# Optimization experiments

Hardware: AMD Instinct MI355X
Metric: run time of the kernel (lower is better)

Reference implementation:

```python
import jax, jax.numpy as jnp
import numpy as np

E = 200_000       # num edges
A = 1_000_000     # num angle triplets
H = 128           # hidden_dim
BD = 8            # bilinear_dim
NR = 6            # num_radial_basis
NS = 7            # num_spherical_basis
MIN = 128         # message_in_dim
N_BEFORE = 1
N_AFTER = 2


def setup_inputs() -> dict:
    key = jax.random.key(0)
    ks = jax.random.split(key, 24)
    s = 0.05
    inp = {
        "distance_representation": jax.random.normal(ks[0], (E, NR), jnp.float32),
        "angle_representation": jax.random.normal(ks[1], (A, NS, NR), jnp.float32),
        "message": jax.random.normal(ks[2], (E, MIN), jnp.float32),
        "angle_index": jax.random.randint(ks[3], (2, A), 0, E),
        # parameters (stored as [in, out]; torch Linear applies x @ W.T)
        "W_dist": jax.random.normal(ks[4], (NR, H), jnp.float32) * s,
        "W_angle": jax.random.normal(ks[5], (NS * NR, BD), jnp.float32) * s,
        "W_src": jax.random.normal(ks[6], (MIN, H), jnp.float32) * s,
        "b_src": jnp.zeros((H,), jnp.float32),
        "W_tgt": jax.random.normal(ks[7], (MIN, H), jnp.float32) * s,
        "b_tgt": jnp.zeros((H,), jnp.float32),
        "W_bil": jax.random.normal(ks[8], (H, BD, H), jnp.float32) * (2.0 / H),
        "res_before_W": jax.random.normal(ks[9], (N_BEFORE, 2, H, H), jnp.float32) * s,
        "res_before_b": jnp.zeros((N_BEFORE, 2, H), jnp.float32),
        "W_skip": jax.random.normal(ks[10], (H, MIN), jnp.float32) * s,
        "b_skip": jnp.zeros((MIN,), jnp.float32),
        "res_after_W": jax.random.normal(ks[11], (N_AFTER, 2, MIN, MIN), jnp.float32) * s,
        "res_after_b": jnp.zeros((N_AFTER, 2, MIN), jnp.float32),
    }
    return inp


def _residual(x, Ws, bs, act):
    # x + act(L2(act(L1(x))))
    h = act(x @ Ws[0] + bs[0])
    h = act(h @ Ws[1] + bs[1])
    return x + h


def reference(distance_representation, angle_representation, message, angle_index,
              W_dist, W_angle, W_src, b_src, W_tgt, b_tgt, W_bil,
              res_before_W, res_before_b, W_skip, b_skip,
              res_after_W, res_after_b):
    act = jax.nn.silu
    num_edges = message.shape[0]
    num_angles = angle_index.shape[-1]

    d = distance_representation @ W_dist                       # [E, H]
    a = angle_representation.reshape(num_angles, -1) @ W_angle  # [A, BD]

    src_e, tgt_e = angle_index[0], angle_index[1]
    sm = message[src_e] @ W_src + b_src                        # [A, H] gather + linear
    sm = sm * d[tgt_e]                                         # [A, H]
    sm = jnp.einsum('ab,ah,ibh->ai', a, sm, W_bil)             # [A, H] bilinear

    agg = jax.ops.segment_sum(sm, tgt_e, num_segments=num_edges)  # [E, H] scatter-add

    x0 = message
    x = agg + (message @ W_tgt + b_tgt)
    for i in range(res_before_W.shape[0]):
        x = _residual(x, res_before_W[i], res_before_b[i], act)
    x = act(x @ W_skip + b_skip) + x0
    for i in range(res_after_W.shape[0]):
        x = _residual(x, res_after_W[i], res_after_b[i], act)
    return x
```

## Files before the change

### kernel.cpp

```cpp
#include <hip/hip_runtime.h>
#include <hip/hip_fp16.h>
#include <stdint.h>

#define E_N 200000
#define A_N 1000000

typedef short s16x8 __attribute__((ext_vector_type(8)));
typedef short s16x4 __attribute__((ext_vector_type(4)));
typedef float f32x4 __attribute__((ext_vector_type(4)));
typedef uint32_t u32x4 __attribute__((ext_vector_type(4)));
typedef uint32_t u32x2 __attribute__((ext_vector_type(2)));
typedef _Float16 f16x8 __attribute__((ext_vector_type(8)));

__device__ __forceinline__ ushort f2bf(float f) {
  uint32_t x = __float_as_uint(f);
  uint32_t r = x + 0x7FFFu + ((x >> 16) & 1u);
  return (ushort)(r >> 16);
}

__device__ __forceinline__ ushort f2h(float f) {
  return __half_as_ushort(__float2half(f));
}

__device__ __forceinline__ uint32_t cvtpk(float lo, float hi) {
  uint32_t r;
  asm("v_cvt_pk_bf16_f32 %0, %1, %2" : "=v"(r) : "v"(lo), "v"(hi));
  return r;
}

__device__ __forceinline__ uint32_t pkmul(uint32_t a, uint32_t b) {
  uint32_t r;
  asm("v_pk_mul_f16 %0, %1, %2" : "=v"(r) : "v"(a), "v"(b));
  return r;
}

__device__ __forceinline__ float silu_f(float v) {
  return v * (1.0f / (1.0f + __expf(-v)));
}

__device__ __forceinline__ int swz(int row, int h) {
  return row * 128 + (h ^ ((row & 7) << 3));
}

__device__ __forceinline__ int sws(int r, int c) {
  return r * 64 + ((c & 63) ^ ((r & 7) << 3));
}

__device__ __forceinline__ void exchCtoB(ushort* scw, int r15, int hi,
                                         const f32x4* xv, s16x8* st) {
  u32x2 pk[8];
#pragma unroll
  for (int nt = 0; nt < 8; nt++) {
    pk[nt][0] = cvtpk(xv[nt][0], xv[nt][1]);
    pk[nt][1] = cvtpk(xv[nt][2], xv[nt][3]);
  }
#pragma unroll
  for (int nt = 0; nt < 4; nt++)
    *(u32x2*)&scw[sws(r15, nt * 16 + hi * 4)] = pk[nt];
#pragma unroll
  for (int k = 0; k < 2; k++)
    st[k] = *(const s16x8*)&scw[sws(r15, k * 32 + hi * 8)];
#pragma unroll
  for (int nt = 4; nt < 8; nt++)
    *(u32x2*)&scw[sws(r15, nt * 16 + hi * 4)] = pk[nt];
#pragma unroll
  for (int k = 2; k < 4; k++)
    st[k] = *(const s16x8*)&scw[sws(r15, k * 32 + hi * 8)];
}

__device__ __forceinline__ void exchBtoC(ushort* scw, int r15, int hi,
                                         const s16x8* stv, u32x2* mc) {
#pragma unroll
  for (int k = 0; k < 2; k++)
    *(s16x8*)&scw[sws(r15, k * 32 + hi * 8)] = stv[k];
#pragma unroll
  for (int nt = 0; nt < 4; nt++)
    mc[nt] = *(const u32x2*)&scw[sws(r15, nt * 16 + hi * 4)];
#pragma unroll
  for (int k = 2; k < 4; k++)
    *(s16x8*)&scw[sws(r15, k * 32 + hi * 8)] = stv[k];
#pragma unroll
  for (int nt = 4; nt < 8; nt++)
    mc[nt] = *(const u32x2*)&scw[sws(r15, nt * 16 + hi * 4)];
}

__global__ __launch_bounds__(256) void k_prep(
    const float* __restrict__ Wbil, const float* __restrict__ Wsrc,
    const float* __restrict__ Wtgt, const float* __restrict__ WresB,
    const float* __restrict__ Wskip, const float* __restrict__ WresA,
    const float* __restrict__ bsrc, const float* __restrict__ btgt,
    const float* __restrict__ bresB, const float* __restrict__ bskip,
    const float* __restrict__ bresA,
    ushort* __restrict__ wg_bil, ushort* __restrict__ wg_lin,
    float* __restrict__ bias_tab) {
  int tid = blockIdx.x * 256 + threadIdx.x;
  if (tid < 8 * 16384) {
    int b = tid >> 14, r = tid & 16383;
    int i = r >> 7, h = r & 127;
    wg_bil[b * 16384 + swz(i, h)] = f2h(Wbil[(i * 8 + b) * 128 + h]);
    return;
  }
  tid -= 8 * 16384;
  if (tid < 9 * 16384) {
    int s = tid >> 14, r = tid & 16383;
    int c = r >> 7, h = r & 127;
    const float* src;
    switch (s) {
      case 0: src = Wsrc; break;
      case 1: src = Wtgt; break;
      case 2: src = WresB; break;
      case 3: src = WresB + 16384; break;
      case 4: src = Wskip; break;
      case 5: src = WresA; break;
      case 6: src = WresA + 16384; break;
      case 7: src = WresA + 32768; break;
      default: src = WresA + 49152; break;
    }
    wg_lin[s * 16384 + swz(c, h)] = f2bf(src[h * 128 + c]);
    return;
  }
  tid -= 9 * 16384;
  if (tid < 9 * 128) {
    int s = tid >> 7, c = tid & 127;
    const float* src;
    switch (s) {
      case 0: src = bsrc; break;
      case 1: src = btgt; break;
      case 2: src = bresB; break;
      case 3: src = bresB + 128; break;
      case 4: src = bskip; break;
      case 5: src = bresA; break;
      case 6: src = bresA + 128; break;
      case 7: src = bresA + 256; break;
      default: src = bresA + 384; break;
    }
    bias_tab[s * 128 + c] = src[c];
  }
}

__global__ __launch_bounds__(256) void k_hist(const int* __restrict__ aidx,
                                              int* __restrict__ cnt) {
  int i = blockIdx.x * 256 + threadIdx.x;
  if (i < A_N) atomicAdd(&cnt[aidx[A_N + i]], 1);
}

__global__ __launch_bounds__(256) void k_scan1(const int* __restrict__ cnt,
                                               int* __restrict__ excl,
                                               int* __restrict__ bsum) {
  __shared__ int s[256];
  int t = threadIdx.x;
  int base = blockIdx.x * 1024 + t * 4;
  int v[4];
#pragma unroll
  for (int j = 0; j < 4; j++) v[j] = (base + j < E_N) ? cnt[base + j] : 0;
  int sum = v[0] + v[1] + v[2] + v[3];
  s[t] = sum;
  __syncthreads();
#pragma unroll
  for (int d = 1; d < 256; d <<= 1) {
    int x = (t >= d) ? s[t - d] : 0;
    __syncthreads();
    s[t] += x;
    __syncthreads();
  }
  int run = s[t] - sum;
#pragma unroll
  for (int j = 0; j < 4; j++) {
    if (base + j < E_N) excl[base + j] = run;
    run += v[j];
  }
  if (t == 255) bsum[blockIdx.x] = s[255];
}

__global__ __launch_bounds__(256) void k_scan2(int* __restrict__ bsum, int nb) {
  __shared__ int s[256];
  int t = threadIdx.x;
  int orig = (t < nb) ? bsum[t] : 0;
  s[t] = orig;
  __syncthreads();
#pragma unroll
  for (int d = 1; d < 256; d <<= 1) {
    int x = (t >= d) ? s[t - d] : 0;
    __syncthreads();
    s[t] += x;
    __syncthreads();
  }
  if (t < nb) bsum[t] = s[t] - orig;
}

__global__ __launch_bounds__(256) void k_scan3(const int* __restrict__ excl,
                                               const int* __restrict__ bsum,
                                               int* __restrict__ cursor) {
  int t = threadIdx.x;
  int base = blockIdx.x * 1024 + t * 4;
  int add = bsum[blockIdx.x];
#pragma unroll
  for (int j = 0; j < 4; j++)
    if (base + j < E_N) cursor[base + j] = excl[base + j] + add;
}

__global__ __launch_bounds__(256) void k_scatter(const int* __restrict__ aidx,
                                                 int* __restrict__ cursor,
                                                 int* __restrict__ perm,
                                                 int* __restrict__ ste) {
  int i = blockIdx.x * 256 + threadIdx.x;
  if (i < A_N) {
    int te = aidx[A_N + i];
    int pos = atomicAdd(&cursor[te], 1);
    perm[pos] = i;
    ste[pos] = te;
  }
}

__global__ __launch_bounds__(256) void k_angle(const float* __restrict__ ang,
                                               const float* __restrict__ Wang,
                                               float* __restrict__ a_ws) {
  __shared__ float rows[128 * 42];
  __shared__ float wbuf[42 * 8];
  int t = threadIdx.x;
  int tile0 = blockIdx.x * 128;
  int nrows = A_N - tile0; if (nrows > 128) nrows = 128;
  if (nrows == 128) {
    const f32x4* src = (const f32x4*)(ang + (size_t)tile0 * 42);
    f32x4* dst = (f32x4*)rows;
    for (int k = t; k < 1344; k += 256) dst[k] = src[k];
  } else {
    int cnt = nrows * 42;
    for (int k = t; k < cnt; k += 256) rows[k] = ang[(size_t)tile0 * 42 + k];
  }
  for (int k = t; k < 336; k += 256) wbuf[k] = Wang[k];
  __syncthreads();
  int row = t >> 1, half = t & 1;
  if (row < nrows) {
    float a0 = 0.f, a1 = 0.f, a2 = 0.f, a3 = 0.f;
    const float* rp = &rows[row * 42];
    const float* wp = &wbuf[half * 4];
#pragma unroll
    for (int k = 0; k < 42; k++) {
      float v = rp[k];
      a0 += v * wp[k * 8 + 0]; a1 += v * wp[k * 8 + 1];
      a2 += v * wp[k * 8 + 2]; a3 += v * wp[k * 8 + 3];
    }
    f32x4 o; o.x = a0; o.y = a1; o.z = a2; o.w = a3;
    *(f32x4*)&a_ws[(tile0 + row) * 8 + half * 4] = o;
  }
}

__global__ __launch_bounds__(256) void k_dist(const float* __restrict__ dist,
                                              const float* __restrict__ Wd,
                                              ushort* __restrict__ dtab) {
  __shared__ float w[6 * 128];
  int t = threadIdx.x;
  for (int k = t; k < 768; k += 256) w[k] = Wd[k];
  __syncthreads();
  int gid = blockIdx.x * 256 + t;
  int e = gid >> 2, q = gid & 3;
  if (e >= E_N) return;
  float dv[6];
#pragma unroll
  for (int r = 0; r < 6; r++) dv[r] = dist[e * 6 + r];
#pragma unroll
  for (int j = 0; j < 32; j += 4) {
    int c = q * 32 + j;
    s16x4 o;
#pragma unroll
    for (int jj = 0; jj < 4; jj++) {
      float s = 0.f;
#pragma unroll
      for (int r = 0; r < 6; r++) s += dv[r] * w[r * 128 + c + jj];
      o[jj] = (short)f2h(s);
    }
    *(s16x4*)&dtab[e * 128 + c] = o;
  }
}

__global__ __launch_bounds__(512) void k_srcm(const float* __restrict__ msg,
                                              const ushort* __restrict__ wg_lin,
                                              const float* __restrict__ bias_tab,
                                              ushort* __restrict__ srcm) {
  __shared__ ushort xb[128 * 128];
  __shared__ ushort wb[16384];
  __shared__ float bias[128];
  int t = threadIdx.x;
  int tile0 = blockIdx.x * 128;
  const f32x4 Z4 = {0.f, 0.f, 0.f, 0.f};
  for (int off = t * 8; off < 16384; off += 4096)
    *(s16x8*)&wb[off] = *(const s16x8*)&wg_lin[off];
  if (t < 128) bias[t] = bias_tab[t];
  {
    int row = t >> 2, l = t & 3;
    int grow = tile0 + row;
#pragma unroll
    for (int j = 0; j < 8; j++) {
      int h = l * 32 + j * 4;
      s16x4 o; o[0] = 0; o[1] = 0; o[2] = 0; o[3] = 0;
      if (grow < E_N) {
        f32x4 v = *(const f32x4*)&msg[(size_t)grow * 128 + h];
        o[0] = (short)f2bf(v.x); o[1] = (short)f2bf(v.y);
        o[2] = (short)f2bf(v.z); o[3] = (short)f2bf(v.w);
      }
      *(s16x4*)&xb[swz(row, h)] = o;
    }
  }
  __syncthreads();
  int w = t >> 6, lane = t & 63;
  int rbase = w * 16;
  int arow = rbase + (lane & 15);
  int k0 = (lane >> 4) * 8;
  int r0 = (lane >> 4) * 4;
  f32x4 acc[8];
#pragma unroll
  for (int k = 0; k < 4; k++) {
    s16x8 af = *(const s16x8*)&xb[swz(arow, k * 32 + k0)];
#pragma unroll
    for (int nt = 0; nt < 8; nt++) {
      s16x8 bf = *(const s16x8*)&wb[swz(nt * 16 + (lane & 15), k * 32 + k0)];
      acc[nt] = __builtin_amdgcn_mfma_f32_16x16x32_bf16(af, bf, k == 0 ? Z4 : acc[nt], 0, 0, 0);
    }
  }
#pragma unroll
  for (int nt = 0; nt < 8; nt++) {
    int col = nt * 16 + (lane & 15);
    float bv = bias[col];
#pragma unroll
    for (int r = 0; r < 4; r++) {
      int grow = tile0 + rbase + r0 + r;
      if (grow < E_N) srcm[(size_t)grow * 128 + col] = f2h(acc[nt][r] + bv);
    }
  }
}

__global__ __launch_bounds__(256, 3) void k_bil(const int* __restrict__ aidx,
                                                const ushort* __restrict__ srcm,
                                                const ushort* __restrict__ dtab,
                                                const float* __restrict__ a_ws,
                                                const ushort* __restrict__ wg_bil,
                                                const int* __restrict__ perm,
                                                const int* __restrict__ ste,
                                                float* __restrict__ agg) {
  __shared__ ushort wb[16384];
  int t = threadIdx.x;
  int lane = t & 63, w = t >> 6;
  int bid = blockIdx.x;
  int xcd = bid & 7, jj0 = bid >> 3;
  int swb = (xcd < 5 ? xcd * 977 : 5 * 977 + (xcd - 5) * 976) + jj0;
  int tile0 = swb * 128;
  int mb = w * 32;
  int r15 = lane & 15, hi = lane >> 4;
  int k0 = hi * 8;
  int r0 = hi * 4;
  const f32x4 Z4 = {0.f, 0.f, 0.f, 0.f};

  {
    const ushort* gs = wg_bil + w * 4096 + lane * 8;
    ushort* ls = &wb[w * 4096];
#pragma unroll
    for (int i = 0; i < 8; i++)
      __builtin_amdgcn_global_load_lds(
          (const __attribute__((address_space(1))) void*)(gs + i * 512),
          (__attribute__((address_space(3))) void*)(ls + i * 512), 16, 0, 0);
  }

  u32x4 smv[2][4];
  uint32_t avd[2][8];
  int teo[2][4];
#pragma unroll
  for (int mt = 0; mt < 2; mt++) {
    int grow = tile0 + mb + mt * 16 + r15;
    int ok = (grow < A_N);
    int ga = ok ? perm[grow] : 0;
    int se = ok ? aidx[ga] : 0;
    int te = ok ? ste[grow] : 0;
    if (ok) {
      f32x4 a0 = *(const f32x4*)&a_ws[(size_t)ga * 8];
      f32x4 a1 = *(const f32x4*)&a_ws[(size_t)ga * 8 + 4];
#pragma unroll
      for (int j = 0; j < 4; j++) {
        uint32_t h0 = f2h(a0[j]), h1 = f2h(a1[j]);
        avd[mt][j] = (h0 << 16) | h0;
        avd[mt][4 + j] = (h1 << 16) | h1;
      }
    } else {
#pragma unroll
      for (int j = 0; j < 8; j++) avd[mt][j] = 0u;
    }
#pragma unroll
    for (int k = 0; k < 4; k++) {
      u32x4 sv = *(const u32x4*)&srcm[(size_t)se * 128 + k * 32 + k0];
      u32x4 dv = *(const u32x4*)&dtab[(size_t)te * 128 + k * 32 + k0];
#pragma unroll
      for (int j = 0; j < 4; j++) smv[mt][k][j] = pkmul(sv[j], dv[j]);
    }
#pragma unroll
    for (int r = 0; r < 4; r++) {
      int orow = tile0 + mb + mt * 16 + r0 + r;
      teo[mt][r] = (orow < A_N) ? ste[orow] : 0;
    }
  }

  f32x4 OUT[2][8];
#pragma unroll
  for (int mt = 0; mt < 2; mt++)
#pragma unroll
    for (int nt = 0; nt < 8; nt++) OUT[mt][nt] = Z4;

  __syncthreads();

#pragma unroll
  for (int b = 0; b < 8; b++) {
    uint32_t a0b = avd[0][b], a1b = avd[1][b];
    __builtin_amdgcn_s_setprio(1);
#pragma unroll
    for (int k = 0; k < 4; k++) {
      u32x4 p0, p1;
#pragma unroll
      for (int j = 0; j < 4; j++) {
        p0[j] = pkmul(smv[0][k][j], a0b);
        p1[j] = pkmul(smv[1][k][j], a1b);
      }
      f16x8 af0 = __builtin_bit_cast(f16x8, p0);
      f16x8 af1 = __builtin_bit_cast(f16x8, p1);
#pragma unroll
      for (int nt = 0; nt < 8; nt++) {
        f16x8 bf = *(const f16x8*)&wb[swz(nt * 16 + r15, k * 32 + k0)];
        OUT[0][nt] = __builtin_amdgcn_mfma_f32_16x16x32_f16(af0, bf, OUT[0][nt], 0, 0, 0);
        OUT[1][nt] = __builtin_amdgcn_mfma_f32_16x16x32_f16(af1, bf, OUT[1][nt], 0, 0, 0);
      }
    }
    __builtin_amdgcn_s_setprio(0);
    if (b < 7) {
      __syncthreads();
      const ushort* gs = wg_bil + (b + 1) * 16384 + w * 4096 + lane * 8;
      ushort* ls = &wb[w * 4096];
#pragma unroll
      for (int i = 0; i < 8; i++)
        __builtin_amdgcn_global_load_lds(
            (const __attribute__((address_space(1))) void*)(gs + i * 512),
            (__attribute__((address_space(3))) void*)(ls + i * 512), 16, 0, 0);
      __syncthreads();
    }
  }

#pragma unroll
  for (int mt = 0; mt < 2; mt++) {
    float acc[8];
    int cte = teo[mt][0];
#pragma unroll
    for (int nt = 0; nt < 8; nt++) acc[nt] = OUT[mt][nt][0];
#pragma unroll
    for (int r = 1; r < 4; r++) {
      int nte = teo[mt][r];
      if (nte == cte) {
#pragma unroll
        for (int nt = 0; nt < 8; nt++) acc[nt] += OUT[mt][nt][r];
      } else {
        float* base = &agg[(size_t)cte * 128];
#pragma unroll
        for (int nt = 0; nt < 8; nt++)
          unsafeAtomicAdd(base + nt * 16 + r15, acc[nt]);
        cte = nte;
#pragma unroll
        for (int nt = 0; nt < 8; nt++) acc[nt] = OUT[mt][nt][r];
      }
    }
    float* base = &agg[(size_t)cte * 128];
#pragma unroll
    for (int nt = 0; nt < 8; nt++)
      unsafeAtomicAdd(base + nt * 16 + r15, acc[nt]);
  }
}

__global__ __launch_bounds__(512) void k_postA(const float* __restrict__ msg,
                                               const float* __restrict__ agg,
                                               const ushort* __restrict__ wg_lin,
                                               const float* __restrict__ bias_tab,
                                               ushort* __restrict__ xmid) {
  __shared__ ushort wb[4][16384];
  __shared__ ushort sc[8][1024];
  __shared__ float bias[4][128];
  int t = threadIdx.x;
  int lane = t & 63, w = t >> 6;
  int r15 = lane & 15, hi = lane >> 4;
  ushort* scw = &sc[w][0];
  const f32x4 Z4 = {0.f, 0.f, 0.f, 0.f};

#pragma unroll
  for (int s = 0; s < 4; s++) {
    const ushort* gs = wg_lin + (s + 1) * 16384 + t * 8;
    ushort* ls = &wb[s][t * 8];
#pragma unroll
    for (int i = 0; i < 4; i++)
      __builtin_amdgcn_global_load_lds(
          (const __attribute__((address_space(1))) void*)(gs + i * 4096),
          (__attribute__((address_space(3))) void*)(ls + i * 4096), 16, 0, 0);
  }
  if (t < 128) {
#pragma unroll
    for (int s = 0; s < 4; s++) bias[s][t] = bias_tab[(s + 1) * 128 + t];
  }
  __syncthreads();

#pragma unroll 1
  for (int tb = blockIdx.x; tb < 1563; tb += 256) {
    int r = tb * 128 + w * 16 + r15;
    bool ok = r < E_N;
    size_t gb = (size_t)r * 128;

    s16x8 st[4], mg[4];
#pragma unroll
    for (int k = 0; k < 4; k++) {
      f32x4 v0 = Z4, v1 = Z4;
      if (ok) {
        v0 = *(const f32x4*)&msg[gb + k * 32 + hi * 8];
        v1 = *(const f32x4*)&msg[gb + k * 32 + hi * 8 + 4];
      }
      u32x4 p;
      p[0] = cvtpk(v0.x, v0.y); p[1] = cvtpk(v0.z, v0.w);
      p[2] = cvtpk(v1.x, v1.y); p[3] = cvtpk(v1.z, v1.w);
      st[k] = __builtin_bit_cast(s16x8, p);
      mg[k] = st[k];
    }
    f32x4 ag[8];
#pragma unroll
    for (int nt = 0; nt < 8; nt++)
      ag[nt] = ok ? *(const f32x4*)&agg[gb + nt * 16 + hi * 4] : Z4;

    f32x4 xr[8], xv[8], C[8];

#pragma unroll
    for (int k = 0; k < 4; k++)
#pragma unroll
      for (int nt = 0; nt < 8; nt++) {
        s16x8 af = *(const s16x8*)&wb[0][swz(nt * 16 + r15, k * 32 + hi * 8)];
        C[nt] = __builtin_amdgcn_mfma_f32_16x16x32_bf16(af, st[k], k == 0 ? ag[nt] : C[nt], 0, 0, 0);
      }
#pragma unroll
    for (int nt = 0; nt < 8; nt++) {
      f32x4 bv = *(const f32x4*)&bias[0][nt * 16 + hi * 4];
#pragma unroll
      for (int q = 0; q < 4; q++) xv[nt][q] = C[nt][q] + bv[q];
      xr[nt] = xv[nt];
    }
    exchCtoB(scw, r15, hi, xv, st);

#pragma unroll
    for (int k = 0; k < 4; k++)
#pragma unroll
      for (int nt = 0; nt < 8; nt++) {
        s16x8 af = *(const s16x8*)&wb[1][swz(nt * 16 + r15, k * 32 + hi * 8)];
        C[nt] = __builtin_amdgcn_mfma_f32_16x16x32_bf16(af, st[k], k == 0 ? Z4 : C[nt], 0, 0, 0);
      }
#pragma unroll
    for (int nt = 0; nt < 8; nt++) {
      f32x4 bv = *(const f32x4*)&bias[1][nt * 16 + hi * 4];
#pragma unroll
      for (int q = 0; q < 4; q++) xv[nt][q] = silu_f(C[nt][q] + bv[q]);
    }
    exchCtoB(scw, r15, hi, xv, st);

#pragma unroll
    for (int k = 0; k < 4; k++)
#pragma unroll
      for (int nt = 0; nt < 8; nt++) {
        s16x8 af = *(const s16x8*)&wb[2][swz(nt * 16 + r15, k * 32 + hi * 8)];
        C[nt] = __builtin_amdgcn_mfma_f32_16x16x32_bf16(af, st[k], k == 0 ? Z4 : C[nt], 0, 0, 0);
      }
#pragma unroll
    for (int nt = 0; nt < 8; nt++) {
      f32x4 bv = *(const f32x4*)&bias[2][nt * 16 + hi * 4];
#pragma unroll
      for (int q = 0; q < 4; q++) xv[nt][q] = xr[nt][q] + silu_f(C[nt][q] + bv[q]);
    }
    exchCtoB(scw, r15, hi, xv, st);

#pragma unroll
    for (int k = 0; k < 4; k++)
#pragma unroll
      for (int nt = 0; nt < 8; nt++) {
        s16x8 af = *(const s16x8*)&wb[3][swz(nt * 16 + r15, k * 32 + hi * 8)];
        C[nt] = __builtin_amdgcn_mfma_f32_16x16x32_bf16(af, st[k], k == 0 ? Z4 : C[nt], 0, 0, 0);
      }
    u32x2 mc[8];
    exchBtoC(scw, r15, hi, mg, mc);
#pragma unroll
    for (int nt = 0; nt < 8; nt++) {
      f32x4 bv = *(const f32x4*)&bias[3][nt * 16 + hi * 4];
      f32x4 m0;
      m0[0] = __uint_as_float(mc[nt][0] << 16);
      m0[1] = __uint_as_float(mc[nt][0] & 0xffff0000u);
      m0[2] = __uint_as_float(mc[nt][1] << 16);
      m0[3] = __uint_as_float(mc[nt][1] & 0xffff0000u);
      u32x2 pk;
      float o0 = silu_f(C[nt][0] + bv[0]) + m0[0];
      float o1 = silu_f(C[nt][1] + bv[1]) + m0[1];
      float o2 = silu_f(C[nt][2] + bv[2]) + m0[2];
      float o3 = silu_f(C[nt][3] + bv[3]) + m0[3];
      pk[0] = cvtpk(o0, o1);
      pk[1] = cvtpk(o2, o3);
      if (ok) *(u32x2*)&xmid[gb + nt * 16 + hi * 4] = pk;
    }
  }
}

__global__ __launch_bounds__(512) void k_postB(const ushort* __restrict__ xmid,
                                               const ushort* __restrict__ wg_lin,
                                               const float* __restrict__ bias_tab,
                                               float* __restrict__ xout) {
  __shared__ ushort wb[4][16384];
  __shared__ ushort sc[8][1024];
  __shared__ float bias[4][128];
  int t = threadIdx.x;
  int lane = t & 63, w = t >> 6;
  int r15 = lane & 15, hi = lane >> 4;
  ushort* scw = &sc[w][0];
  const f32x4 Z4 = {0.f, 0.f, 0.f, 0.f};

#pragma unroll
  for (int s = 0; s < 4; s++) {
    const ushort* gs = wg_lin + (s + 5) * 16384 + t * 8;
    ushort* ls = &wb[s][t * 8];
#pragma unroll
    for (int i = 0; i < 4; i++)
      __builtin_amdgcn_global_load_lds(
          (const __attribute__((address_space(1))) void*)(gs + i * 4096),
          (__attribute__((address_space(3))) void*)(ls + i * 4096), 16, 0, 0);
  }
  if (t < 128) {
#pragma unroll
    for (int s = 0; s < 4; s++) bias[s][t] = bias_tab[(s + 5) * 128 + t];
  }
  __syncthreads();

#pragma unroll 1
  for (int tb = blockIdx.x; tb < 1563; tb += 256) {
    int r = tb * 128 + w * 16 + r15;
    bool ok = r < E_N;
    size_t gb = (size_t)r * 128;

    s16x8 st[4];
#pragma unroll
    for (int k = 0; k < 4; k++) {
      s16x8 z; u32x4 zz; zz[0] = 0; zz[1] = 0; zz[2] = 0; zz[3] = 0;
      z = __builtin_bit_cast(s16x8, zz);
      st[k] = ok ? *(const s16x8*)&xmid[gb + k * 32 + hi * 8] : z;
    }
    u32x2 mc[8];
    exchBtoC(scw, r15, hi, st, mc);
    f32x4 xr[8], xv[8], C[8];
#pragma unroll
    for (int nt = 0; nt < 8; nt++) {
      xr[nt][0] = __uint_as_float(mc[nt][0] << 16);
      xr[nt][1] = __uint_as_float(mc[nt][0] & 0xffff0000u);
      xr[nt][2] = __uint_as_float(mc[nt][1] << 16);
      xr[nt][3] = __uint_as_float(mc[nt][1] & 0xffff0000u);
    }

#pragma unroll
    for (int k = 0; k < 4; k++)
#pragma unroll
      for (int nt = 0; nt < 8; nt++) {
        s16x8 af = *(const s16x8*)&wb[0][swz(nt * 16 + r15, k * 32 + hi * 8)];
        C[nt] = __builtin_amdgcn_mfma_f32_16x16x32_bf16(af, st[k], k == 0 ? Z4 : C[nt], 0, 0, 0);
      }
#pragma unroll
    for (int nt = 0; nt < 8; nt++) {
      f32x4 bv = *(const f32x4*)&bias[0][nt * 16 + hi * 4];
#pragma unroll
      for (int q = 0; q < 4; q++) xv[nt][q] = silu_f(C[nt][q] + bv[q]);
    }
    exchCtoB(scw, r15, hi, xv, st);

#pragma unroll
    for (int k = 0; k < 4; k++)
#pragma unroll
      for (int nt = 0; nt < 8; nt++) {
        s16x8 af = *(const s16x8*)&wb[1][swz(nt * 16 + r15, k * 32 + hi * 8)];
        C[nt] = __builtin_amdgcn_mfma_f32_16x16x32_bf16(af, st[k], k == 0 ? Z4 : C[nt], 0, 0, 0);
      }
#pragma unroll
    for (int nt = 0; nt < 8; nt++) {
      f32x4 bv = *(const f32x4*)&bias[1][nt * 16 + hi * 4];
#pragma unroll
      for (int q = 0; q < 4; q++) xv[nt][q] = xr[nt][q] + silu_f(C[nt][q] + bv[q]);
      xr[nt] = xv[nt];
    }
    exchCtoB(scw, r15, hi, xv, st);

#pragma unroll
    for (int k = 0; k < 4; k++)
#pragma unroll
      for (int nt = 0; nt < 8; nt++) {
        s16x8 af = *(const s16x8*)&wb[2][swz(nt * 16 + r15, k * 32 + hi * 8)];
        C[nt] = __builtin_amdgcn_mfma_f32_16x16x32_bf16(af, st[k], k == 0 ? Z4 : C[nt], 0, 0, 0);
      }
#pragma unroll
    for (int nt = 0; nt < 8; nt++) {
      f32x4 bv = *(const f32x4*)&bias[2][nt * 16 + hi * 4];
#pragma unroll
      for (int q = 0; q < 4; q++) xv[nt][q] = silu_f(C[nt][q] + bv[q]);
    }
    exchCtoB(scw, r15, hi, xv, st);

#pragma unroll
    for (int k = 0; k < 4; k++)
#pragma unroll
      for (int nt = 0; nt < 8; nt++) {
        s16x8 af = *(const s16x8*)&wb[3][swz(nt * 16 + r15, k * 32 + hi * 8)];
        C[nt] = __builtin_amdgcn_mfma_f32_16x16x32_bf16(af, st[k], k == 0 ? Z4 : C[nt], 0, 0, 0);
      }
#pragma unroll
    for (int nt = 0; nt < 8; nt++) {
      f32x4 bv = *(const f32x4*)&bias[3][nt * 16 + hi * 4];
      f32x4 o;
#pragma unroll
      for (int q = 0; q < 4; q++) o[q] = xr[nt][q] + silu_f(C[nt][q] + bv[q]);
      if (ok) *(f32x4*)&xout[gb + nt * 16 + hi * 4] = o;
    }
  }
}

extern "C" void kernel_launch(void* const* d_in, const int* in_sizes, int n_in,
                              void* d_out, int out_size, void* d_ws, size_t ws_size,
                              hipStream_t stream) {
  const float* dist  = (const float*)d_in[0];
  const float* ang   = (const float*)d_in[1];
  const float* msg   = (const float*)d_in[2];
  const int*   aidx  = (const int*)d_in[3];
  const float* Wd    = (const float*)d_in[4];
  const float* Wang  = (const float*)d_in[5];
  const float* Wsrc  = (const float*)d_in[6];
  const float* bsrc  = (const float*)d_in[7];
  const float* Wtgt  = (const float*)d_in[8];
  const float* btgt  = (const float*)d_in[9];
  const float* Wbil  = (const float*)d_in[10];
  const float* WresB = (const float*)d_in[11];
  const float* bresB = (const float*)d_in[12];
  const float* Wskip = (const float*)d_in[13];
  const float* bskip = (const float*)d_in[14];
  const float* WresA = (const float*)d_in[15];
  const float* bresA = (const float*)d_in[16];

  char* ws = (char*)d_ws;
  ushort* srcm_f16 = (ushort*)(ws + 0);
  ushort* dtab_f16 = (ushort*)(ws + 51200000LL);
  float*  a_ws     = (float*)(ws + 102400000LL);
  ushort* wg_bil   = (ushort*)(ws + 134400000LL);
  ushort* wg_lin   = (ushort*)(ws + 134662144LL);
  float*  bias_tab = (float*)(ws + 134957056LL);
  int*    cnt      = (int*)(ws + 134961664LL);
  int*    cursor   = (int*)(ws + 135761664LL);
  int*    excl     = (int*)(ws + 136561664LL);
  int*    bsum     = (int*)(ws + 137361664LL);
  int*    perm     = (int*)(ws + 137362688LL);
  int*    ste      = (int*)(ws + 141362688LL);
  ushort* xmid     = (ushort*)(ws + 145362688LL);
  float*  agg      = (float*)d_out;

  (void)in_sizes; (void)n_in; (void)out_size; (void)ws_size;

  const int NSCAN = (E_N + 1023) / 1024;

  hipMemsetAsync(d_out, 0, (size_t)E_N * 128 * 4, stream);
  hipMemsetAsync(cnt, 0, (size_t)E_N * 4, stream);
  k_prep<<<1093, 256, 0, stream>>>(Wbil, Wsrc, Wtgt, WresB, Wskip, WresA,
                                   bsrc, btgt, bresB, bskip, bresA,
                                   wg_bil, wg_lin, bias_tab);
  k_hist<<<3907, 256, 0, stream>>>(aidx, cnt);
  k_scan1<<<NSCAN, 256, 0, stream>>>(cnt, excl, bsum);
  k_scan2<<<1, 256, 0, stream>>>(bsum, NSCAN);
  k_scan3<<<NSCAN, 256, 0, stream>>>(excl, bsum, cursor);
  k_scatter<<<3907, 256, 0, stream>>>(aidx, cursor, perm, ste);
  k_angle<<<7813, 256, 0, stream>>>(ang, Wang, a_ws);
  k_dist<<<3125, 256, 0, stream>>>(dist, Wd, dtab_f16);
  k_srcm<<<1563, 512, 0, stream>>>(msg, wg_lin, bias_tab, srcm_f16);
  k_bil<<<7813, 256, 0, stream>>>(aidx, srcm_f16, dtab_f16, a_ws, wg_bil,
                                  perm, ste, agg);
  k_postA<<<256, 512, 0, stream>>>(msg, agg, wg_lin, bias_tab, xmid);
  k_postB<<<256, 512, 0, stream>>>(xmid, wg_lin, bias_tab, (float*)d_out);
}
```

Baseline: 795.2 us.

## Pre-sort angle coefficients and source indices into tgt-sorted order before bilinear

The scatter kernel now also writes the source edge index in sorted order. A new k_asort kernel gathers the angle projection through perm and stores it pre-converted to packed fp16 in sorted order. k_bil then reads sse and a_srt contiguously instead of doing the perm→aidx→a_ws dependent gathers, loads ste with vector reads, and drops the XCD block swizzle. This adds an extra kernel and roughly 36 MB of extra traffic in exchange for shorter dependent-load chains in the main kernel.

```diff
diff --git a/kernel.cpp b/kernel.cpp
--- a/kernel.cpp
+++ b/kernel.cpp
@@ -10,6 +10,7 @@
 typedef float f32x4 __attribute__((ext_vector_type(4)));
 typedef uint32_t u32x4 __attribute__((ext_vector_type(4)));
 typedef uint32_t u32x2 __attribute__((ext_vector_type(2)));
+typedef int i32x4 __attribute__((ext_vector_type(4)));
 typedef _Float16 f16x8 __attribute__((ext_vector_type(8)));
 
 __device__ __forceinline__ ushort f2bf(float f) {
@@ -202,13 +203,16 @@
 __global__ __launch_bounds__(256) void k_scatter(const int* __restrict__ aidx,
                                                  int* __restrict__ cursor,
                                                  int* __restrict__ perm,
-                                                 int* __restrict__ ste) {
+                                                 int* __restrict__ ste,
+                                                 int* __restrict__ sse) {
   int i = blockIdx.x * 256 + threadIdx.x;
   if (i < A_N) {
     int te = aidx[A_N + i];
+    int se = aidx[i];
     int pos = atomicAdd(&cursor[te], 1);
     perm[pos] = i;
     ste[pos] = te;
+    sse[pos] = se;
   }
 }
 
@@ -244,6 +248,25 @@
     f32x4 o; o.x = a0; o.y = a1; o.z = a2; o.w = a3;
     *(f32x4*)&a_ws[(tile0 + row) * 8 + half * 4] = o;
   }
+}
+
+__global__ __launch_bounds__(256) void k_asort(const int* __restrict__ perm,
+                                               const float* __restrict__ a_ws,
+                                               u32x4* __restrict__ a_srt) {
+  int i = blockIdx.x * 256 + threadIdx.x;
+  if (i >= A_N) return;
+  int ga = perm[i];
+  f32x4 a0 = *(const f32x4*)&a_ws[(size_t)ga * 8];
+  f32x4 a1 = *(const f32x4*)&a_ws[(size_t)ga * 8 + 4];
+  u32x4 o0, o1;
+#pragma unroll
+  for (int j = 0; j < 4; j++) {
+    uint32_t h0 = f2h(a0[j]), h1 = f2h(a1[j]);
+    o0[j] = (h0 << 16) | h0;
+    o1[j] = (h1 << 16) | h1;
+  }
+  a_srt[(size_t)i * 2] = o0;
+  a_srt[(size_t)i * 2 + 1] = o1;
 }
 
 __global__ __launch_bounds__(256) void k_dist(const float* __restrict__ dist,
@@ -330,21 +353,17 @@
   }
 }
 
-__global__ __launch_bounds__(256, 3) void k_bil(const int* __restrict__ aidx,
+__global__ __launch_bounds__(256, 3) void k_bil(const int* __restrict__ sse,
                                                 const ushort* __restrict__ srcm,
                                                 const ushort* __restrict__ dtab,
-                                                const float* __restrict__ a_ws,
+                                                const u32x4* __restrict__ a_srt,
                                                 const ushort* __restrict__ wg_bil,
-                                                const int* __restrict__ perm,
                                                 const int* __restrict__ ste,
                                                 float* __restrict__ agg) {
   __shared__ ushort wb[16384];
   int t = threadIdx.x;
   int lane = t & 63, w = t >> 6;
-  int bid = blockIdx.x;
-  int xcd = bid & 7, jj0 = bid >> 3;
-  int swb = (xcd < 5 ? xcd * 977 : 5 * 977 + (xcd - 5) * 976) + jj0;
-  int tile0 = swb * 128;
+  int tile0 = blockIdx.x * 128;
   int mb = w * 32;
   int r15 = lane & 15, hi = lane >> 4;
   int k0 = hi * 8;
@@ -368,18 +387,13 @@
   for (int mt = 0; mt < 2; mt++) {
     int grow = tile0 + mb + mt * 16 + r15;
     int ok = (grow < A_N);
-    int ga = ok ? perm[grow] : 0;
-    int se = ok ? aidx[ga] : 0;
+    int se = ok ? sse[grow] : 0;
     int te = ok ? ste[grow] : 0;
     if (ok) {
-      f32x4 a0 = *(const f32x4*)&a_ws[(size_t)ga * 8];
-      f32x4 a1 = *(const f32x4*)&a_ws[(size_t)ga * 8 + 4];
-#pragma unroll
-      for (int j = 0; j < 4; j++) {
-        uint32_t h0 = f2h(a0[j]), h1 = f2h(a1[j]);
-        avd[mt][j] = (h0 << 16) | h0;
-        avd[mt][4 + j] = (h1 << 16) | h1;
-      }
+      u32x4 o0 = a_srt[(size_t)grow * 2];
+      u32x4 o1 = a_srt[(size_t)grow * 2 + 1];
+#pragma unroll
+      for (int j = 0; j < 4; j++) { avd[mt][j] = o0[j]; avd[mt][4 + j] = o1[j]; }
     } else {
 #pragma unroll
       for (int j = 0; j < 8; j++) avd[mt][j] = 0u;
@@ -391,10 +405,15 @@
 #pragma unroll
       for (int j = 0; j < 4; j++) smv[mt][k][j] = pkmul(sv[j], dv[j]);
     }
-#pragma unroll
-    for (int r = 0; r < 4; r++) {
-      int orow = tile0 + mb + mt * 16 + r0 + r;
-      teo[mt][r] = (orow < A_N) ? ste[orow] : 0;
+    int orow0 = tile0 + mb + mt * 16 + r0;
+    if (orow0 + 3 < A_N) {
+      i32x4 tq = *(const i32x4*)&ste[orow0];
+#pragma unroll
+      for (int r = 0; r < 4; r++) teo[mt][r] = tq[r];
+    } else {
+#pragma unroll
+      for (int r = 0; r < 4; r++)
+        teo[mt][r] = (orow0 + r < A_N) ? ste[orow0 + r] : 0;
     }
   }
 
@@ -754,6 +773,8 @@
   int*    perm     = (int*)(ws + 137362688LL);
   int*    ste      = (int*)(ws + 141362688LL);
   ushort* xmid     = (ushort*)(ws + 145362688LL);
+  int*    sse      = (int*)(ws + 196562688LL);
+  u32x4*  a_srt    = (u32x4*)(ws + 200562688LL);
   float*  agg      = (float*)d_out;
 
   (void)in_sizes; (void)n_in; (void)out_size; (void)ws_size;
@@ -769,12 +790,13 @@
   k_scan1<<<NSCAN, 256, 0, stream>>>(cnt, excl, bsum);
   k_scan2<<<1, 256, 0, stream>>>(bsum, NSCAN);
   k_scan3<<<NSCAN, 256, 0, stream>>>(excl, bsum, cursor);
-  k_scatter<<<3907, 256, 0, stream>>>(aidx, cursor, perm, ste);
+  k_scatter<<<3907, 256, 0, stream>>>(aidx, cursor, perm, ste, sse);
   k_angle<<<7813, 256, 0, stream>>>(ang, Wang, a_ws);
+  k_asort<<<3907, 256, 0, stream>>>(perm, a_ws, a_srt);
   k_dist<<<3125, 256, 0, stream>>>(dist, Wd, dtab_f16);
   k_srcm<<<1563, 512, 0, stream>>>(msg, wg_lin, bias_tab, srcm_f16);
-  k_bil<<<7813, 256, 0, stream>>>(aidx, srcm_f16, dtab_f16, a_ws, wg_bil,
-                                  perm, ste, agg);
+  k_bil<<<7813, 256, 0, stream>>>(sse, srcm_f16, dtab_f16, a_srt, wg_bil,
+                                  ste, agg);
   k_postA<<<256, 512, 0, stream>>>(msg, agg, wg_lin, bias_tab, xmid);
   k_postB<<<256, 512, 0, stream>>>(xmid, wg_lin, bias_tab, (float*)d_out);
 }
```

Result: no change. 800.1 us (+0.6%).
